# Kernel optimization log

Measured on AMD Instinct MI355X. Metric: run time of the kernel, lower is better.

Reference implementation:

```python
import jax, jax.numpy as jnp
import numpy as np

K = 3          # attention window (kernel_size)
PAD = 1        # padding
C_IN = 256
C_OUT = 512    # final_channel
N_SPECIES, N_FAMILY, N_ORDER = 64500, 510, 100


def setup_inputs() -> dict:
    key = jax.random.key(0)
    ks = jax.random.split(key, 16)
    B, H, W = 4, 64, 64
    std = 0.01  # per torch.nn.init.normal_(std=0.01)
    inp = {
        "x": jax.random.normal(ks[0], (B, C_IN, H, W), jnp.float32),
        "wq": jax.random.normal(ks[1], (C_OUT, C_IN), jnp.float32) * std,
        "bq": jnp.zeros((C_OUT,), jnp.float32),
        "wk": jax.random.normal(ks[2], (C_OUT, C_IN), jnp.float32) * std,
        "bk": jnp.zeros((C_OUT,), jnp.float32),
        "wv": jax.random.normal(ks[3], (C_OUT, C_IN), jnp.float32) * std,
        "bv": jnp.zeros((C_OUT,), jnp.float32),
        "rel_h": jax.random.normal(ks[4], (C_OUT // 2, K), jnp.float32),
        "rel_w": jax.random.normal(ks[5], (C_OUT // 2, K), jnp.float32),
        "w_species": jax.random.normal(ks[6], (N_SPECIES, C_OUT), jnp.float32) * std,
        "b_species": jnp.zeros((N_SPECIES,), jnp.float32),
        "w_family": jax.random.normal(ks[7], (N_FAMILY, C_OUT), jnp.float32) * std,
        "b_family": jnp.zeros((N_FAMILY,), jnp.float32),
        "w_order": jax.random.normal(ks[8], (N_ORDER, C_OUT), jnp.float32) * std,
        "b_order": jnp.zeros((N_ORDER,), jnp.float32),
    }
    return inp


def _patches(t, H, W):
    # t: padded [B, C, H+2, W+2] -> [B, C, H, W, K, K] (unfold order: kh then kw)
    return jnp.stack([
        jnp.stack([t[:, :, i:i + H, j:j + W] for j in range(K)], axis=-1)
        for i in range(K)], axis=-2)


def _attention_conv(x, wq, bq, wk, bk, wv, bv, rel_h, rel_w):
    B, _, H, W = x.shape
    q = jnp.einsum('oc,bchw->bohw', wq, x) + bq[None, :, None, None]
    k = jnp.einsum('oc,bchw->bohw', wk, x) + bk[None, :, None, None]
    v = jnp.einsum('oc,bchw->bohw', wv, x) + bv[None, :, None, None]
    pad = ((0, 0), (0, 0), (PAD, PAD), (PAD, PAD))
    kp = _patches(jnp.pad(k, pad), H, W)                       # [B,C,H,W,K,K]
    vp = _patches(jnp.pad(v, pad), H, W).reshape(B, C_OUT, H, W, K * K)
    half = C_OUT // 2
    kp = jnp.concatenate([
        kp[:, :half] + rel_h[None, :, None, None, :, None],    # rel over kh
        kp[:, half:] + rel_w[None, :, None, None, None, :],    # rel over kw
    ], axis=1).reshape(B, C_OUT, H, W, K * K)
    attn = jax.nn.softmax(q[..., None] * kp, axis=-1)          # per-channel softmax over window
    return jnp.einsum('bchwk,bchwk->bchw', attn, vp)


def reference(x, wq, bq, wk, bk, wv, bv, rel_h, rel_w,
              w_species, b_species, w_family, b_family, w_order, b_order):
    att = jax.nn.relu(_attention_conv(x, wq, bq, wk, bk, wv, bv, rel_h, rel_w))
    pooled = att.mean(axis=(2, 3))                             # AdaptiveAvgPool2d((1,1)) -> [B, 512]
    sp = pooled @ w_species.T + b_species
    fa = pooled @ w_family.T + b_family
    od = pooled @ w_order.T + b_order
    # concatenated per-level logits (species | family | order)
    return jnp.concatenate([sp, fa, od], axis=1)
```

## Files before the change

### kernel.cpp

```cpp
#include <hip/hip_runtime.h>
#include <stdint.h>

#define HW    4096
#define CIN   256
#define COUT  512
#define NSPE  64500
#define NFAM  510
#define NORD  100
#define NOUT  65110

typedef __attribute__((ext_vector_type(8))) short bf16x8;
typedef __attribute__((ext_vector_type(4))) float f32x4;
typedef __attribute__((address_space(3))) uint32_t lds_u32;
typedef __attribute__((address_space(1))) const uint32_t glob_u32;

__device__ __forceinline__ short f32_to_bf16(float f) {
    uint32_t u = __float_as_uint(f);
    u += 0x7fffu + ((u >> 16) & 1u);
    return (short)(u >> 16);
}
__device__ __forceinline__ float bf16_to_f32(unsigned short s) {
    return __uint_as_float(((uint32_t)s) << 16);
}


__global__ __launch_bounds__(256) void convert_w_kernel(
    const float* __restrict__ wq, const float* __restrict__ wk,
    const float* __restrict__ wv, short* __restrict__ Wt)
{
    const int kt = blockIdx.x, mt = blockIdx.y, mat = blockIdx.z;
    const float* __restrict__ W = (mat == 0) ? wq : (mat == 1) ? wk : wv;
    const int t = threadIdx.x;
    const int m = t >> 1;
    short* out = Wt + (((size_t)(mat * 4 + mt) * 8 + kt) << 12);

    union { short s[16]; int4 v[2]; } pk;
    #pragma unroll
    for (int j = 0; j < 16; ++j) {
        int e  = t * 16 + j;
        int sp = (e >> 3) & 3;
        int i  = e & 7;
        int k  = ((sp ^ ((m >> 1) & 3)) << 3) + i;
        pk.s[j] = f32_to_bf16(W[(size_t)(mt * 128 + m) * CIN + kt * 32 + k]);
    }
    int4* dst = (int4*)(out + t * 16);
    dst[0] = pk.v[0];
    dst[1] = pk.v[1];
}

__global__ __launch_bounds__(256) void convert_x_kernel(
    const float* __restrict__ x, short* __restrict__ Xt)
{
    const int kt = blockIdx.x, nt = blockIdx.y, b = blockIdx.z;
    const int t = threadIdx.x;
    __shared__ float lds[32][128];

    #pragma unroll
    for (int j = 0; j < 16; ++j) {
        int idx = j * 256 + t;
        int c = idx >> 7, p = idx & 127;
        lds[c][p] = x[((size_t)b * CIN + kt * 32 + c) * HW + nt * 128 + p];
    }
    __syncthreads();

    const int n = t >> 1;
    short* out = Xt + (((size_t)(b * 32 + nt) * 8 + kt) << 12);
    union { short s[16]; int4 v[2]; } pk;
    #pragma unroll
    for (int j = 0; j < 16; ++j) {
        int e  = t * 16 + j;
        int sp = (e >> 3) & 3;
        int i  = e & 7;
        int k  = ((sp ^ ((n >> 1) & 3)) << 3) + i;
        pk.s[j] = f32_to_bf16(lds[k][n]);
    }
    int4* dst = (int4*)(out + t * 16);
    dst[0] = pk.v[0];
    dst[1] = pk.v[1];
}

__global__ __launch_bounds__(256) void qkv_mfma_kernel(
    const short* __restrict__ Wt, const short* __restrict__ Xt,
    const float* __restrict__ bq, const float* __restrict__ bk,
    const float* __restrict__ bv, short* __restrict__ qkv)
{
    const int nt = blockIdx.x, mt = blockIdx.y, z = blockIdx.z;
    const int mat = z >> 2, b = z & 3;
    const short* At = Wt + (((size_t)(mat * 4 + mt) * 8) << 12);
    const short* Bt = Xt + (((size_t)(b * 32 + nt) * 8) << 12);

    __shared__ __align__(16) short As[2][4096];
    __shared__ __align__(16) short Bs[2][4096];

    const int tid = threadIdx.x, lane = tid & 63, wid = tid >> 6;
    const int wm = wid >> 1, wn = wid & 1;
    const int l15 = lane & 15, sl = lane >> 4;
    const int sw = ((sl ^ ((l15 >> 1) & 3)) << 3);

    f32x4 acc[4][4] = {};

#define STAGE(KT, BUF) do {                                                   \
    _Pragma("unroll")                                                         \
    for (int j = 0; j < 4; ++j) {                                             \
        int li = wid * 4 + j;                                                 \
        if (li < 8)                                                           \
            __builtin_amdgcn_global_load_lds(                                 \
                (glob_u32*)(At + (KT) * 4096 + li * 512 + lane * 8),          \
                (lds_u32*)(&As[BUF][li * 512]), 16, 0, 0);                    \
        else                                                                  \
            __builtin_amdgcn_global_load_lds(                                 \
                (glob_u32*)(Bt + (KT) * 4096 + (li - 8) * 512 + lane * 8),    \
                (lds_u32*)(&Bs[BUF][(li - 8) * 512]), 16, 0, 0);              \
    }                                                                         \
} while (0)

    STAGE(0, 0);
    __syncthreads();

    int buf = 0;
    #pragma unroll 2
    for (int kt = 0; kt < 8; ++kt) {
        if (kt < 7) STAGE(kt + 1, buf ^ 1);

        bf16x8 a[4], bb[4];
        #pragma unroll
        for (int f = 0; f < 4; ++f) {
            int ra = wm * 64 + f * 16 + l15;
            a[f]  = *(const bf16x8*)(&As[buf][ra * 32 + sw]);
            int rb = wn * 64 + f * 16 + l15;
            bb[f] = *(const bf16x8*)(&Bs[buf][rb * 32 + sw]);
        }
        #pragma unroll
        for (int mf = 0; mf < 4; ++mf)
            #pragma unroll
            for (int nf = 0; nf < 4; ++nf)
                acc[mf][nf] = __builtin_amdgcn_mfma_f32_16x16x32_bf16(
                    a[mf], bb[nf], acc[mf][nf], 0, 0, 0);
        __syncthreads();
        buf ^= 1;
    }
#undef STAGE

    const float* bias = (mat == 0) ? bq : (mat == 1) ? bk : bv;
    short* out = qkv + (((size_t)(b * 3 + mat) * COUT + mt * 128) * HW) + nt * 128;
    const int col = lane & 15, g = lane >> 4;
    #pragma unroll
    for (int mf = 0; mf < 4; ++mf) {
        #pragma unroll
        for (int nf = 0; nf < 4; ++nf) {
            #pragma unroll
            for (int r = 0; r < 4; ++r) {
                int m = wm * 64 + mf * 16 + g * 4 + r;
                int n = wn * 64 + nf * 16 + col;
                float val = acc[mf][nf][r] + bias[mt * 128 + m];
                out[(size_t)m * HW + n] = f32_to_bf16(val);
            }
        }
    }
}

__global__ __launch_bounds__(256) void attn_pool_kernel(
    const unsigned short* __restrict__ qkv,
    const float* __restrict__ rel_h, const float* __restrict__ rel_w,
    float* __restrict__ pooled)
{
    const int c = blockIdx.x;
    const int b = blockIdx.y;
    const int tid = threadIdx.x;
    const int h  = tid >> 2;
    const int w0 = (tid & 3) * 16;

    const unsigned short* qc = qkv + ((size_t)(b * 3 + 0) * COUT + c) * HW;
    const unsigned short* kg = qkv + ((size_t)(b * 3 + 1) * COUT + c) * HW;
    const unsigned short* vg = qkv + ((size_t)(b * 3 + 2) * COUT + c) * HW;

    __shared__ float kS[66 * 67];
    __shared__ float vS[66 * 67];

    if (tid < 67) {
        kS[tid] = 0.f;            vS[tid] = 0.f;
        kS[65 * 67 + tid] = 0.f;  vS[65 * 67 + tid] = 0.f;
    }
    if (tid < 64) {
        int r0 = (tid + 1) * 67;
        kS[r0] = 0.f;       vS[r0] = 0.f;
        kS[r0 + 65] = 0.f;  vS[r0 + 65] = 0.f;
    }

    #pragma unroll
    for (int it = 0; it < 2; ++it) {
        int ch = tid + it * 256;
        int y = ch >> 3, xs = (ch & 7) * 8;
        union { int4 v; unsigned short s[8]; } ak, av;
        ak.v = reinterpret_cast<const int4*>(kg)[ch];
        av.v = reinterpret_cast<const int4*>(vg)[ch];
        float* kp = &kS[(y + 1) * 67 + xs + 1];
        float* vp = &vS[(y + 1) * 67 + xs + 1];
        #pragma unroll
        for (int e = 0; e < 8; ++e) {
            kp[e] = bf16_to_f32(ak.s[e]);
            vp[e] = bf16_to_f32(av.s[e]);
        }
    }

    union { unsigned short s[16]; int4 v[2]; } qr;
    qr.v[0] = reinterpret_cast<const int4*>(qc + h * 64 + w0)[0];
    qr.v[1] = reinterpret_cast<const int4*>(qc + h * 64 + w0)[1];
    float qf[16];
    #pragma unroll
    for (int i = 0; i < 16; ++i)
        qf[i] = bf16_to_f32(qr.s[i]) * 1.4426950408889634f;

    const bool isH = (c < 256);
    float r3[3];
    #pragma unroll
    for (int i = 0; i < 3; ++i)
        r3[i] = isH ? rel_h[c * 3 + i] : rel_w[(c - 256) * 3 + i];
    float relv[9];
    #pragma unroll
    for (int kh = 0; kh < 3; ++kh)
        #pragma unroll
        for (int kw = 0; kw < 3; ++kw)
            relv[kh * 3 + kw] = isH ? r3[kh] : r3[kw];

    __syncthreads();

    const float* krow = &kS[h * 67 + w0];
    const float* vrow = &vS[h * 67 + w0];

    float kcw[3][3], vcw[3][3];
    #pragma unroll
    for (int s = 0; s < 2; ++s)
        #pragma unroll
        for (int r = 0; r < 3; ++r) {
            kcw[s][r] = krow[r * 67 + s];
            vcw[s][r] = vrow[r * 67 + s];
        }

    float total = 0.f;
    #pragma unroll
    for (int i = 0; i < 16; ++i) {
        const int s2 = (i + 2) % 3;
        #pragma unroll
        for (int r = 0; r < 3; ++r) {
            kcw[s2][r] = krow[r * 67 + i + 2];
            vcw[s2][r] = vrow[r * 67 + i + 2];
        }
        const float q2 = qf[i];
        float num = 0.f, den = 0.f;
        #pragma unroll
        for (int r = 0; r < 3; ++r)
            #pragma unroll
            for (int dx = 0; dx < 3; ++dx) {
                const int sl = (i + dx) % 3;
                float e = __builtin_exp2f(q2 * (kcw[sl][r] + relv[r * 3 + dx]));
                den += e;
                num = fmaf(e, vcw[sl][r], num);
            }
        total += fmaxf(num * __builtin_amdgcn_rcpf(den), 0.f);
    }

    #pragma unroll
    for (int off = 32; off; off >>= 1) total += __shfl_down(total, off);
    __shared__ float red[4];
    if ((tid & 63) == 0) red[tid >> 6] = total;
    __syncthreads();
    if (tid == 0)
        pooled[b * COUT + c] = (red[0] + red[1] + red[2] + red[3]) * (1.f / 4096.f);
}

__global__ __launch_bounds__(256) void heads_kernel(
    const float* __restrict__ pooled,
    const float* __restrict__ w_sp, const float* __restrict__ b_sp,
    const float* __restrict__ w_fa, const float* __restrict__ b_fa,
    const float* __restrict__ w_or, const float* __restrict__ b_or,
    float* __restrict__ out)
{
    const int lane   = threadIdx.x & 63;
    const int wave   = blockIdx.x * (blockDim.x >> 6) + (threadIdx.x >> 6);
    const int nwaves = gridDim.x * (blockDim.x >> 6);

    float pr[4][8];
    #pragma unroll
    for (int b = 0; b < 4; ++b)
        #pragma unroll
        for (int e = 0; e < 8; ++e)
            pr[b][e] = pooled[b * COUT + lane * 8 + e];

    for (int j = wave; j < NOUT; j += nwaves) {
        const float* __restrict__ wrow;
        float bias;
        if (j < NSPE)            { wrow = w_sp + (size_t)j * COUT;          bias = b_sp[j]; }
        else if (j < NSPE + NFAM){ wrow = w_fa + (size_t)(j - NSPE) * COUT; bias = b_fa[j - NSPE]; }
        else                     { wrow = w_or + (size_t)(j - NSPE - NFAM) * COUT; bias = b_or[j - NSPE - NFAM]; }

        const float4 w0 = reinterpret_cast<const float4*>(wrow)[lane * 2 + 0];
        const float4 w1 = reinterpret_cast<const float4*>(wrow)[lane * 2 + 1];
        const float we[8] = {w0.x, w0.y, w0.z, w0.w, w1.x, w1.y, w1.z, w1.w};

        float a0 = 0.f, a1 = 0.f, a2 = 0.f, a3 = 0.f;
        #pragma unroll
        for (int e = 0; e < 8; ++e) {
            a0 += we[e] * pr[0][e];
            a1 += we[e] * pr[1][e];
            a2 += we[e] * pr[2][e];
            a3 += we[e] * pr[3][e];
        }
        #pragma unroll
        for (int off = 32; off; off >>= 1) {
            a0 += __shfl_down(a0, off);
            a1 += __shfl_down(a1, off);
            a2 += __shfl_down(a2, off);
            a3 += __shfl_down(a3, off);
        }
        if (lane == 0) {
            out[0 * NOUT + j] = a0 + bias;
            out[1 * NOUT + j] = a1 + bias;
            out[2 * NOUT + j] = a2 + bias;
            out[3 * NOUT + j] = a3 + bias;
        }
    }
}

extern "C" void kernel_launch(void* const* d_in, const int* in_sizes, int n_in,
                              void* d_out, int out_size, void* d_ws, size_t ws_size,
                              hipStream_t stream) {
    const float* x     = (const float*)d_in[0];
    const float* wq    = (const float*)d_in[1];
    const float* bq    = (const float*)d_in[2];
    const float* wk    = (const float*)d_in[3];
    const float* bk    = (const float*)d_in[4];
    const float* wv    = (const float*)d_in[5];
    const float* bv    = (const float*)d_in[6];
    const float* rel_h = (const float*)d_in[7];
    const float* rel_w = (const float*)d_in[8];
    const float* w_sp  = (const float*)d_in[9];
    const float* b_sp  = (const float*)d_in[10];
    const float* w_fa  = (const float*)d_in[11];
    const float* b_fa  = (const float*)d_in[12];
    const float* w_or  = (const float*)d_in[13];
    const float* b_or  = (const float*)d_in[14];
    float* out = (float*)d_out;

    short* Wt  = (short*)d_ws;
    short* Xt  = Wt + 393216;
    short* qkv = Xt + 4194304;
    float* pooled = (float*)(qkv + 25165824);

    convert_w_kernel<<<dim3(8, 4, 3), 256, 0, stream>>>(wq, wk, wv, Wt);
    convert_x_kernel<<<dim3(8, 32, 4), 256, 0, stream>>>(x, Xt);
    qkv_mfma_kernel<<<dim3(32, 4, 12), 256, 0, stream>>>(Wt, Xt, bq, bk, bv, qkv);
    attn_pool_kernel<<<dim3(COUT, 4), 256, 0, stream>>>(
        (const unsigned short*)qkv, rel_h, rel_w, pooled);
    heads_kernel<<<dim3(2048), 256, 0, stream>>>(
        pooled, w_sp, b_sp, w_fa, b_fa, w_or, b_or, out);
}
```

Measured before the change: 84.96 us.

## Fuse weight/input conversion kernels and widen QKV GEMM tile to 128x256

Merges the two bf16 conversion kernels into one launch, with grid z selecting either the x transpose or the weight conversion. The QKV MFMA kernel now computes a 128x256 output tile per block, so each warp holds 4x8 accumulators. Each A tile is therefore reused across twice as many columns and the block count halves. Bias values are hoisted into registers before the store loop, and the launch bound requests 2 blocks per CU. The costs are higher register pressure and more LDS per block (48KB), which may reduce occupancy.

```diff
diff --git a/kernel.cpp b/kernel.cpp
--- a/kernel.cpp
+++ b/kernel.cpp
@@ -24,93 +24,98 @@
 }
 
 
-__global__ __launch_bounds__(256) void convert_w_kernel(
+__global__ __launch_bounds__(256) void convert_kernel(
+    const float* __restrict__ x,
     const float* __restrict__ wq, const float* __restrict__ wk,
-    const float* __restrict__ wv, short* __restrict__ Wt)
+    const float* __restrict__ wv,
+    short* __restrict__ Xt, short* __restrict__ Wt)
 {
-    const int kt = blockIdx.x, mt = blockIdx.y, mat = blockIdx.z;
-    const float* __restrict__ W = (mat == 0) ? wq : (mat == 1) ? wk : wv;
-    const int t = threadIdx.x;
-    const int m = t >> 1;
-    short* out = Wt + (((size_t)(mat * 4 + mt) * 8 + kt) << 12);
-
-    union { short s[16]; int4 v[2]; } pk;
-    #pragma unroll
-    for (int j = 0; j < 16; ++j) {
-        int e  = t * 16 + j;
-        int sp = (e >> 3) & 3;
-        int i  = e & 7;
-        int k  = ((sp ^ ((m >> 1) & 3)) << 3) + i;
-        pk.s[j] = f32_to_bf16(W[(size_t)(mt * 128 + m) * CIN + kt * 32 + k]);
-    }
-    int4* dst = (int4*)(out + t * 16);
-    dst[0] = pk.v[0];
-    dst[1] = pk.v[1];
-}
-
-__global__ __launch_bounds__(256) void convert_x_kernel(
-    const float* __restrict__ x, short* __restrict__ Xt)
-{
-    const int kt = blockIdx.x, nt = blockIdx.y, b = blockIdx.z;
     const int t = threadIdx.x;
     __shared__ float lds[32][128];
 
-    #pragma unroll
-    for (int j = 0; j < 16; ++j) {
-        int idx = j * 256 + t;
-        int c = idx >> 7, p = idx & 127;
-        lds[c][p] = x[((size_t)b * CIN + kt * 32 + c) * HW + nt * 128 + p];
-    }
-    __syncthreads();
-
-    const int n = t >> 1;
-    short* out = Xt + (((size_t)(b * 32 + nt) * 8 + kt) << 12);
-    union { short s[16]; int4 v[2]; } pk;
-    #pragma unroll
-    for (int j = 0; j < 16; ++j) {
-        int e  = t * 16 + j;
-        int sp = (e >> 3) & 3;
-        int i  = e & 7;
-        int k  = ((sp ^ ((n >> 1) & 3)) << 3) + i;
-        pk.s[j] = f32_to_bf16(lds[k][n]);
-    }
-    int4* dst = (int4*)(out + t * 16);
-    dst[0] = pk.v[0];
-    dst[1] = pk.v[1];
-}
-
-__global__ __launch_bounds__(256) void qkv_mfma_kernel(
+    if (blockIdx.z < 4) {
+        const int kt = blockIdx.x, nt = blockIdx.y, b = blockIdx.z;
+        #pragma unroll
+        for (int j = 0; j < 16; ++j) {
+            int idx = j * 256 + t;
+            int c = idx >> 7, p = idx & 127;
+            lds[c][p] = x[((size_t)b * CIN + kt * 32 + c) * HW + nt * 128 + p];
+        }
+        __syncthreads();
+
+        const int n = t >> 1;
+        short* out = Xt + (((size_t)(b * 32 + nt) * 8 + kt) << 12);
+        union { short s[16]; int4 v[2]; } pk;
+        #pragma unroll
+        for (int j = 0; j < 16; ++j) {
+            int e  = t * 16 + j;
+            int sp = (e >> 3) & 3;
+            int i  = e & 7;
+            int k  = ((sp ^ ((n >> 1) & 3)) << 3) + i;
+            pk.s[j] = f32_to_bf16(lds[k][n]);
+        }
+        int4* dst = (int4*)(out + t * 16);
+        dst[0] = pk.v[0];
+        dst[1] = pk.v[1];
+    } else {
+        if (blockIdx.y >= 12) return;
+        const int kt = blockIdx.x, mt = blockIdx.y & 3, mat = blockIdx.y >> 2;
+        const float* __restrict__ W = (mat == 0) ? wq : (mat == 1) ? wk : wv;
+        const int m = t >> 1;
+        short* out = Wt + (((size_t)(mat * 4 + mt) * 8 + kt) << 12);
+
+        union { short s[16]; int4 v[2]; } pk;
+        #pragma unroll
+        for (int j = 0; j < 16; ++j) {
+            int e  = t * 16 + j;
+            int sp = (e >> 3) & 3;
+            int i  = e & 7;
+            int k  = ((sp ^ ((m >> 1) & 3)) << 3) + i;
+            pk.s[j] = f32_to_bf16(W[(size_t)(mt * 128 + m) * CIN + kt * 32 + k]);
+        }
+        int4* dst = (int4*)(out + t * 16);
+        dst[0] = pk.v[0];
+        dst[1] = pk.v[1];
+    }
+}
+
+__global__ __launch_bounds__(256, 2) void qkv_mfma_kernel(
     const short* __restrict__ Wt, const short* __restrict__ Xt,
     const float* __restrict__ bq, const float* __restrict__ bk,
     const float* __restrict__ bv, short* __restrict__ qkv)
 {
     const int nt = blockIdx.x, mt = blockIdx.y, z = blockIdx.z;
-    const int mat = z >> 2, b = z & 3;
-    const short* At = Wt + (((size_t)(mat * 4 + mt) * 8) << 12);
-    const short* Bt = Xt + (((size_t)(b * 32 + nt) * 8) << 12);
+    const int b = z / 3, mat = z % 3;
+    const short* At  = Wt + (((size_t)(mat * 4 + mt) * 8) << 12);
+    const short* Bt0 = Xt + (((size_t)(b * 32 + nt * 2) * 8) << 12);
+    const short* Bt1 = Bt0 + 8 * 4096;
 
     __shared__ __align__(16) short As[2][4096];
-    __shared__ __align__(16) short Bs[2][4096];
+    __shared__ __align__(16) short Bs[2][8192];
 
     const int tid = threadIdx.x, lane = tid & 63, wid = tid >> 6;
     const int wm = wid >> 1, wn = wid & 1;
     const int l15 = lane & 15, sl = lane >> 4;
     const int sw = ((sl ^ ((l15 >> 1) & 3)) << 3);
 
-    f32x4 acc[4][4] = {};
+    f32x4 acc[4][8] = {};
 
 #define STAGE(KT, BUF) do {                                                   \
     _Pragma("unroll")                                                         \
-    for (int j = 0; j < 4; ++j) {                                             \
-        int li = wid * 4 + j;                                                 \
+    for (int j = 0; j < 6; ++j) {                                             \
+        int li = wid * 6 + j;                                                 \
         if (li < 8)                                                           \
             __builtin_amdgcn_global_load_lds(                                 \
                 (glob_u32*)(At + (KT) * 4096 + li * 512 + lane * 8),          \
                 (lds_u32*)(&As[BUF][li * 512]), 16, 0, 0);                    \
+        else if (li < 16)                                                     \
+            __builtin_amdgcn_global_load_lds(                                 \
+                (glob_u32*)(Bt0 + (KT) * 4096 + (li - 8) * 512 + lane * 8),   \
+                (lds_u32*)(&Bs[BUF][(li - 8) * 512]), 16, 0, 0);              \
         else                                                                  \
             __builtin_amdgcn_global_load_lds(                                 \
-                (glob_u32*)(Bt + (KT) * 4096 + (li - 8) * 512 + lane * 8),    \
-                (lds_u32*)(&Bs[BUF][(li - 8) * 512]), 16, 0, 0);              \
+                (glob_u32*)(Bt1 + (KT) * 4096 + (li - 16) * 512 + lane * 8),  \
+                (lds_u32*)(&Bs[BUF][4096 + (li - 16) * 512]), 16, 0, 0);      \
     }                                                                         \
 } while (0)
 
@@ -122,18 +127,18 @@
     for (int kt = 0; kt < 8; ++kt) {
         if (kt < 7) STAGE(kt + 1, buf ^ 1);
 
-        bf16x8 a[4], bb[4];
-        #pragma unroll
-        for (int f = 0; f < 4; ++f) {
-            int ra = wm * 64 + f * 16 + l15;
-            a[f]  = *(const bf16x8*)(&As[buf][ra * 32 + sw]);
-            int rb = wn * 64 + f * 16 + l15;
-            bb[f] = *(const bf16x8*)(&Bs[buf][rb * 32 + sw]);
-        }
+        bf16x8 a[4], bb[8];
+        #pragma unroll
+        for (int f = 0; f < 4; ++f)
+            a[f] = *(const bf16x8*)(&As[buf][(wm * 64 + f * 16 + l15) * 32 + sw]);
+        #pragma unroll
+        for (int f = 0; f < 8; ++f)
+            bb[f] = *(const bf16x8*)(&Bs[buf][wn * 4096 + (f * 16 + l15) * 32 + sw]);
+
         #pragma unroll
         for (int mf = 0; mf < 4; ++mf)
             #pragma unroll
-            for (int nf = 0; nf < 4; ++nf)
+            for (int nf = 0; nf < 8; ++nf)
                 acc[mf][nf] = __builtin_amdgcn_mfma_f32_16x16x32_bf16(
                     a[mf], bb[nf], acc[mf][nf], 0, 0, 0);
         __syncthreads();
@@ -142,18 +147,25 @@
 #undef STAGE
 
     const float* bias = (mat == 0) ? bq : (mat == 1) ? bk : bv;
-    short* out = qkv + (((size_t)(b * 3 + mat) * COUT + mt * 128) * HW) + nt * 128;
+    short* out = qkv + (((size_t)(b * 3 + mat) * COUT + mt * 128) * HW) + nt * 256;
     const int col = lane & 15, g = lane >> 4;
+
+    float biasv[4][4];
+    #pragma unroll
+    for (int mf = 0; mf < 4; ++mf)
+        #pragma unroll
+        for (int r = 0; r < 4; ++r)
+            biasv[mf][r] = bias[mt * 128 + wm * 64 + mf * 16 + g * 4 + r];
+
     #pragma unroll
     for (int mf = 0; mf < 4; ++mf) {
         #pragma unroll
-        for (int nf = 0; nf < 4; ++nf) {
+        for (int nf = 0; nf < 8; ++nf) {
             #pragma unroll
             for (int r = 0; r < 4; ++r) {
                 int m = wm * 64 + mf * 16 + g * 4 + r;
-                int n = wn * 64 + nf * 16 + col;
-                float val = acc[mf][nf][r] + bias[mt * 128 + m];
-                out[(size_t)m * HW + n] = f32_to_bf16(val);
+                int n = wn * 128 + nf * 16 + col;
+                out[(size_t)m * HW + n] = f32_to_bf16(acc[mf][nf][r] + biasv[mf][r]);
             }
         }
     }
@@ -347,9 +359,8 @@
     short* qkv = Xt + 4194304;
     float* pooled = (float*)(qkv + 25165824);
 
-    convert_w_kernel<<<dim3(8, 4, 3), 256, 0, stream>>>(wq, wk, wv, Wt);
-    convert_x_kernel<<<dim3(8, 32, 4), 256, 0, stream>>>(x, Xt);
-    qkv_mfma_kernel<<<dim3(32, 4, 12), 256, 0, stream>>>(Wt, Xt, bq, bk, bv, qkv);
+    convert_kernel<<<dim3(8, 32, 5), 256, 0, stream>>>(x, wq, wk, wv, Xt, Wt);
+    qkv_mfma_kernel<<<dim3(16, 4, 12), 256, 0, stream>>>(Wt, Xt, bq, bk, bv, qkv);
     attn_pool_kernel<<<dim3(COUT, 4), 256, 0, stream>>>(
         (const unsigned short*)qkv, rel_h, rel_w, pooled);
     heads_kernel<<<dim3(2048), 256, 0, stream>>>(
```

New measurement: 87.26 us. +2.7%, slower.

## Pipeline batches inside attention blocks with double-buffered LDS and merge convert kernels

Applied to the files above, without the earlier changes.

The attention pooling kernel now processes all four batches for a channel in one block, prefetching the next batch's q/k/v into registers and writing it to a second LDS buffer while the current batch computes. The two fp32-to-bf16 conversion kernels are fused into a single launch to cut launch overhead. This aims to hide global load latency in the attention stage, but it reduces the grid to 512 blocks and doubles LDS use, which lowers occupancy and parallelism.

```diff
diff --git a/kernel.cpp b/kernel.cpp
--- a/kernel.cpp
+++ b/kernel.cpp
@@ -24,59 +24,59 @@
 }
 
 
-__global__ __launch_bounds__(256) void convert_w_kernel(
+__global__ __launch_bounds__(256) void convert_kernel(
+    const float* __restrict__ x,
     const float* __restrict__ wq, const float* __restrict__ wk,
-    const float* __restrict__ wv, short* __restrict__ Wt)
+    const float* __restrict__ wv,
+    short* __restrict__ Xt, short* __restrict__ Wt)
 {
-    const int kt = blockIdx.x, mt = blockIdx.y, mat = blockIdx.z;
-    const float* __restrict__ W = (mat == 0) ? wq : (mat == 1) ? wk : wv;
-    const int t = threadIdx.x;
-    const int m = t >> 1;
-    short* out = Wt + (((size_t)(mat * 4 + mt) * 8 + kt) << 12);
-
-    union { short s[16]; int4 v[2]; } pk;
-    #pragma unroll
-    for (int j = 0; j < 16; ++j) {
-        int e  = t * 16 + j;
-        int sp = (e >> 3) & 3;
-        int i  = e & 7;
-        int k  = ((sp ^ ((m >> 1) & 3)) << 3) + i;
-        pk.s[j] = f32_to_bf16(W[(size_t)(mt * 128 + m) * CIN + kt * 32 + k]);
-    }
-    int4* dst = (int4*)(out + t * 16);
-    dst[0] = pk.v[0];
-    dst[1] = pk.v[1];
-}
-
-__global__ __launch_bounds__(256) void convert_x_kernel(
-    const float* __restrict__ x, short* __restrict__ Xt)
-{
-    const int kt = blockIdx.x, nt = blockIdx.y, b = blockIdx.z;
     const int t = threadIdx.x;
     __shared__ float lds[32][128];
 
-    #pragma unroll
-    for (int j = 0; j < 16; ++j) {
-        int idx = j * 256 + t;
-        int c = idx >> 7, p = idx & 127;
-        lds[c][p] = x[((size_t)b * CIN + kt * 32 + c) * HW + nt * 128 + p];
-    }
-    __syncthreads();
-
-    const int n = t >> 1;
-    short* out = Xt + (((size_t)(b * 32 + nt) * 8 + kt) << 12);
-    union { short s[16]; int4 v[2]; } pk;
-    #pragma unroll
-    for (int j = 0; j < 16; ++j) {
-        int e  = t * 16 + j;
-        int sp = (e >> 3) & 3;
-        int i  = e & 7;
-        int k  = ((sp ^ ((n >> 1) & 3)) << 3) + i;
-        pk.s[j] = f32_to_bf16(lds[k][n]);
-    }
-    int4* dst = (int4*)(out + t * 16);
-    dst[0] = pk.v[0];
-    dst[1] = pk.v[1];
+    if (blockIdx.z < 4) {
+        const int kt = blockIdx.x, nt = blockIdx.y, b = blockIdx.z;
+        #pragma unroll
+        for (int j = 0; j < 16; ++j) {
+            int idx = j * 256 + t;
+            int c = idx >> 7, p = idx & 127;
+            lds[c][p] = x[((size_t)b * CIN + kt * 32 + c) * HW + nt * 128 + p];
+        }
+        __syncthreads();
+
+        const int n = t >> 1;
+        short* out = Xt + (((size_t)(b * 32 + nt) * 8 + kt) << 12);
+        union { short s[16]; int4 v[2]; } pk;
+        #pragma unroll
+        for (int j = 0; j < 16; ++j) {
+            int e  = t * 16 + j;
+            int sp = (e >> 3) & 3;
+            int i  = e & 7;
+            int k  = ((sp ^ ((n >> 1) & 3)) << 3) + i;
+            pk.s[j] = f32_to_bf16(lds[k][n]);
+        }
+        int4* dst = (int4*)(out + t * 16);
+        dst[0] = pk.v[0];
+        dst[1] = pk.v[1];
+    } else {
+        if (blockIdx.y >= 12) return;
+        const int kt = blockIdx.x, mt = blockIdx.y & 3, mat = blockIdx.y >> 2;
+        const float* __restrict__ W = (mat == 0) ? wq : (mat == 1) ? wk : wv;
+        const int m = t >> 1;
+        short* out = Wt + (((size_t)(mat * 4 + mt) * 8 + kt) << 12);
+
+        union { short s[16]; int4 v[2]; } pk;
+        #pragma unroll
+        for (int j = 0; j < 16; ++j) {
+            int e  = t * 16 + j;
+            int sp = (e >> 3) & 3;
+            int i  = e & 7;
+            int k  = ((sp ^ ((m >> 1) & 3)) << 3) + i;
+            pk.s[j] = f32_to_bf16(W[(size_t)(mt * 128 + m) * CIN + kt * 32 + k]);
+        }
+        int4* dst = (int4*)(out + t * 16);
+        dst[0] = pk.v[0];
+        dst[1] = pk.v[1];
+    }
 }
 
 __global__ __launch_bounds__(256) void qkv_mfma_kernel(
@@ -165,51 +165,26 @@
     float* __restrict__ pooled)
 {
     const int c = blockIdx.x;
-    const int b = blockIdx.y;
     const int tid = threadIdx.x;
     const int h  = tid >> 2;
     const int w0 = (tid & 3) * 16;
 
-    const unsigned short* qc = qkv + ((size_t)(b * 3 + 0) * COUT + c) * HW;
-    const unsigned short* kg = qkv + ((size_t)(b * 3 + 1) * COUT + c) * HW;
-    const unsigned short* vg = qkv + ((size_t)(b * 3 + 2) * COUT + c) * HW;
-
-    __shared__ float kS[66 * 67];
-    __shared__ float vS[66 * 67];
-
-    if (tid < 67) {
-        kS[tid] = 0.f;            vS[tid] = 0.f;
-        kS[65 * 67 + tid] = 0.f;  vS[65 * 67 + tid] = 0.f;
-    }
-    if (tid < 64) {
-        int r0 = (tid + 1) * 67;
-        kS[r0] = 0.f;       vS[r0] = 0.f;
-        kS[r0 + 65] = 0.f;  vS[r0 + 65] = 0.f;
-    }
-
-    #pragma unroll
-    for (int it = 0; it < 2; ++it) {
-        int ch = tid + it * 256;
-        int y = ch >> 3, xs = (ch & 7) * 8;
-        union { int4 v; unsigned short s[8]; } ak, av;
-        ak.v = reinterpret_cast<const int4*>(kg)[ch];
-        av.v = reinterpret_cast<const int4*>(vg)[ch];
-        float* kp = &kS[(y + 1) * 67 + xs + 1];
-        float* vp = &vS[(y + 1) * 67 + xs + 1];
-        #pragma unroll
-        for (int e = 0; e < 8; ++e) {
-            kp[e] = bf16_to_f32(ak.s[e]);
-            vp[e] = bf16_to_f32(av.s[e]);
-        }
-    }
-
-    union { unsigned short s[16]; int4 v[2]; } qr;
-    qr.v[0] = reinterpret_cast<const int4*>(qc + h * 64 + w0)[0];
-    qr.v[1] = reinterpret_cast<const int4*>(qc + h * 64 + w0)[1];
-    float qf[16];
-    #pragma unroll
-    for (int i = 0; i < 16; ++i)
-        qf[i] = bf16_to_f32(qr.s[i]) * 1.4426950408889634f;
+    __shared__ float kS[2][66 * 67];
+    __shared__ float vS[2][66 * 67];
+    __shared__ float red[4][4];
+
+    #pragma unroll
+    for (int bu = 0; bu < 2; ++bu) {
+        if (tid < 67) {
+            kS[bu][tid] = 0.f;            vS[bu][tid] = 0.f;
+            kS[bu][65 * 67 + tid] = 0.f;  vS[bu][65 * 67 + tid] = 0.f;
+        }
+        if (tid < 64) {
+            int r0 = (tid + 1) * 67;
+            kS[bu][r0] = 0.f;       vS[bu][r0] = 0.f;
+            kS[bu][r0 + 65] = 0.f;  vS[bu][r0 + 65] = 0.f;
+        }
+    }
 
     const bool isH = (c < 256);
     float r3[3];
@@ -223,50 +198,106 @@
         for (int kw = 0; kw < 3; ++kw)
             relv[kh * 3 + kw] = isH ? r3[kh] : r3[kw];
 
+    const int y0 = tid >> 3,         xs0 = (tid & 7) * 8;
+    const int y1 = (tid + 256) >> 3, xs1 = ((tid + 256) & 7) * 8;
+
+    int4 krg0, krg1, vrg0, vrg1, qn0, qn1;
+#define LOADB(B) do {                                                         \
+    const unsigned short* kg_ = qkv + ((size_t)((B) * 3 + 1) * COUT + c) * HW;\
+    const unsigned short* vg_ = qkv + ((size_t)((B) * 3 + 2) * COUT + c) * HW;\
+    const unsigned short* qc_ = qkv + ((size_t)((B) * 3 + 0) * COUT + c) * HW;\
+    krg0 = reinterpret_cast<const int4*>(kg_)[tid];                           \
+    krg1 = reinterpret_cast<const int4*>(kg_)[tid + 256];                     \
+    vrg0 = reinterpret_cast<const int4*>(vg_)[tid];                           \
+    vrg1 = reinterpret_cast<const int4*>(vg_)[tid + 256];                     \
+    qn0  = reinterpret_cast<const int4*>(qc_ + h * 64 + w0)[0];               \
+    qn1  = reinterpret_cast<const int4*>(qc_ + h * 64 + w0)[1];               \
+} while (0)
+
+#define WRITEB(BUF) do {                                                      \
+    union { int4 v; unsigned short s[8]; } ak_, av_;                          \
+    ak_.v = krg0; av_.v = vrg0;                                               \
+    _Pragma("unroll")                                                         \
+    for (int e = 0; e < 8; ++e) {                                             \
+        kS[BUF][(y0 + 1) * 67 + xs0 + 1 + e] = bf16_to_f32(ak_.s[e]);         \
+        vS[BUF][(y0 + 1) * 67 + xs0 + 1 + e] = bf16_to_f32(av_.s[e]);         \
+    }                                                                         \
+    ak_.v = krg1; av_.v = vrg1;                                               \
+    _Pragma("unroll")                                                         \
+    for (int e = 0; e < 8; ++e) {                                             \
+        kS[BUF][(y1 + 1) * 67 + xs1 + 1 + e] = bf16_to_f32(ak_.s[e]);         \
+        vS[BUF][(y1 + 1) * 67 + xs1 + 1 + e] = bf16_to_f32(av_.s[e]);         \
+    }                                                                         \
+} while (0)
+
+    LOADB(0);
+    WRITEB(0);
+
+    #pragma unroll
+    for (int b = 0; b < 4; ++b) {
+        const int buf = b & 1;
+
+        float qf[16];
+        {
+            union { int4 v[2]; unsigned short s[16]; } qu;
+            qu.v[0] = qn0; qu.v[1] = qn1;
+            #pragma unroll
+            for (int i = 0; i < 16; ++i)
+                qf[i] = bf16_to_f32(qu.s[i]) * 1.4426950408889634f;
+        }
+
+        if (b < 3) LOADB(b + 1);
+
+        __syncthreads();
+
+        const float* krow = &kS[buf][h * 67 + w0];
+        const float* vrow = &vS[buf][h * 67 + w0];
+
+        float kcw[3][3], vcw[3][3];
+        #pragma unroll
+        for (int s = 0; s < 2; ++s)
+            #pragma unroll
+            for (int r = 0; r < 3; ++r) {
+                kcw[s][r] = krow[r * 67 + s];
+                vcw[s][r] = vrow[r * 67 + s];
+            }
+
+        float total = 0.f;
+        #pragma unroll
+        for (int i = 0; i < 16; ++i) {
+            const int s2 = (i + 2) % 3;
+            #pragma unroll
+            for (int r = 0; r < 3; ++r) {
+                kcw[s2][r] = krow[r * 67 + i + 2];
+                vcw[s2][r] = vrow[r * 67 + i + 2];
+            }
+            const float q2 = qf[i];
+            float num = 0.f, den = 0.f;
+            #pragma unroll
+            for (int r = 0; r < 3; ++r)
+                #pragma unroll
+                for (int dx = 0; dx < 3; ++dx) {
+                    const int sl = (i + dx) % 3;
+                    float e = __builtin_exp2f(q2 * (kcw[sl][r] + relv[r * 3 + dx]));
+                    den += e;
+                    num = fmaf(e, vcw[sl][r], num);
+                }
+            total += fmaxf(num * __builtin_amdgcn_rcpf(den), 0.f);
+        }
+
+        if (b < 3) WRITEB(buf ^ 1);
+
+        #pragma unroll
+        for (int off = 32; off; off >>= 1) total += __shfl_down(total, off);
+        if ((tid & 63) == 0) red[b][tid >> 6] = total;
+    }
+#undef LOADB
+#undef WRITEB
+
     __syncthreads();
-
-    const float* krow = &kS[h * 67 + w0];
-    const float* vrow = &vS[h * 67 + w0];
-
-    float kcw[3][3], vcw[3][3];
-    #pragma unroll
-    for (int s = 0; s < 2; ++s)
-        #pragma unroll
-        for (int r = 0; r < 3; ++r) {
-            kcw[s][r] = krow[r * 67 + s];
-            vcw[s][r] = vrow[r * 67 + s];
-        }
-
-    float total = 0.f;
-    #pragma unroll
-    for (int i = 0; i < 16; ++i) {
-        const int s2 = (i + 2) % 3;
-        #pragma unroll
-        for (int r = 0; r < 3; ++r) {
-            kcw[s2][r] = krow[r * 67 + i + 2];
-            vcw[s2][r] = vrow[r * 67 + i + 2];
-        }
-        const float q2 = qf[i];
-        float num = 0.f, den = 0.f;
-        #pragma unroll
-        for (int r = 0; r < 3; ++r)
-            #pragma unroll
-            for (int dx = 0; dx < 3; ++dx) {
-                const int sl = (i + dx) % 3;
-                float e = __builtin_exp2f(q2 * (kcw[sl][r] + relv[r * 3 + dx]));
-                den += e;
-                num = fmaf(e, vcw[sl][r], num);
-            }
-        total += fmaxf(num * __builtin_amdgcn_rcpf(den), 0.f);
-    }
-
-    #pragma unroll
-    for (int off = 32; off; off >>= 1) total += __shfl_down(total, off);
-    __shared__ float red[4];
-    if ((tid & 63) == 0) red[tid >> 6] = total;
-    __syncthreads();
-    if (tid == 0)
-        pooled[b * COUT + c] = (red[0] + red[1] + red[2] + red[3]) * (1.f / 4096.f);
+    if (tid < 4)
+        pooled[tid * COUT + c] =
+            (red[tid][0] + red[tid][1] + red[tid][2] + red[tid][3]) * (1.f / 4096.f);
 }
 
 __global__ __launch_bounds__(256) void heads_kernel(
@@ -347,10 +378,9 @@
     short* qkv = Xt + 4194304;
     float* pooled = (float*)(qkv + 25165824);
 
-    convert_w_kernel<<<dim3(8, 4, 3), 256, 0, stream>>>(wq, wk, wv, Wt);
-    convert_x_kernel<<<dim3(8, 32, 4), 256, 0, stream>>>(x, Xt);
+    convert_kernel<<<dim3(8, 32, 5), 256, 0, stream>>>(x, wq, wk, wv, Xt, Wt);
     qkv_mfma_kernel<<<dim3(32, 4, 12), 256, 0, stream>>>(Wt, Xt, bq, bk, bv, qkv);
-    attn_pool_kernel<<<dim3(COUT, 4), 256, 0, stream>>>(
+    attn_pool_kernel<<<dim3(COUT), 256, 0, stream>>>(
         (const unsigned short*)qkv, rel_h, rel_w, pooled);
     heads_kernel<<<dim3(2048), 256, 0, stream>>>(
         pooled, w_sp, b_sp, w_fa, b_fa, w_or, b_or, out);
```

New measurement: 83.35 us. No clear change (-1.9%).
